# Kernel tuning notes

Hardware: AMD Instinct MI355X
Metric: run time of the kernel (lower is better)

Reference implementation:

```python
import jax, jax.numpy as jnp
import numpy as np
import math

D = 2048
NH = 16
DH = D // NH
LAT = D // 4
B, S = 2, 2048
EPS = 1e-5


def _ln(x, g, b):
    m = jnp.mean(x, axis=-1, keepdims=True)
    v = jnp.mean((x - m) ** 2, axis=-1, keepdims=True)
    return (x - m) * jax.lax.rsqrt(v + EPS) * g + b


def setup_inputs() -> dict:
    key = jax.random.key(0)
    ks = jax.random.split(key, 12)
    p = lambda k, shape: 0.01 * jax.random.normal(k, shape, dtype=jnp.float32)
    return {
        "x": jax.random.normal(ks[0], (B, S, D), dtype=jnp.float32),
        "W_dq": p(ks[1], (D, LAT)),
        "W_uq": p(ks[2], (LAT, D)),
        "q_ln_g": jnp.ones((LAT,), jnp.float32),
        "q_ln_b": jnp.zeros((LAT,), jnp.float32),
        "W_dkv": p(ks[3], (D, LAT)),
        "W_ukv": p(ks[4], (LAT, 2 * D)),
        "kv_ln_g": jnp.ones((LAT,), jnp.float32),
        "kv_ln_b": jnp.zeros((LAT,), jnp.float32),
        "W_o": p(ks[5], (D, D)),
        "norm1_g": jnp.ones((D,), jnp.float32),
        "norm1_b": jnp.zeros((D,), jnp.float32),
        "norm2_g": jnp.ones((D,), jnp.float32),
        "norm2_b": jnp.zeros((D,), jnp.float32),
        "fc1_w": p(ks[6], (4 * D, D)),
        "fc1_b": jnp.zeros((4 * D,), jnp.float32),
        "fc2_w": p(ks[7], (D, 4 * D)),
        "fc2_b": jnp.zeros((D,), jnp.float32),
    }


def reference(x, W_dq, W_uq, q_ln_g, q_ln_b, W_dkv, W_ukv, kv_ln_g, kv_ln_b,
              W_o, norm1_g, norm1_b, norm2_g, norm2_b, fc1_w, fc1_b, fc2_w, fc2_b):
    normed = _ln(x, norm1_g, norm1_b)

    # --- RopelessMLA attention ---
    cq = _ln(normed @ W_dq, q_ln_g, q_ln_b)          # [B,S,LAT]
    Q = cq @ W_uq                                     # [B,S,D]
    ckv = _ln(normed @ W_dkv, kv_ln_g, kv_ln_b)       # [B,S,LAT]
    KV = ckv @ W_ukv                                  # [B,S,2D]
    K, V = KV[..., :D], KV[..., D:]

    q = Q.reshape(B, S, NH, DH)
    k = K.reshape(B, S, NH, DH)
    v = V.reshape(B, S, NH, DH)

    qkt = jnp.einsum("bqhd,bkhd->bhqk", q, k) / math.sqrt(float(DH))
    mask = jnp.tril(jnp.ones((S, S), dtype=qkt.dtype))  # causal, past_length=0
    qkt = qkt * mask
    qkt = jnp.where(qkt == 0.0, -jnp.inf, qkt)  # faithful to original zero->-inf trick
    attn = jax.nn.softmax(qkt, axis=-1)
    o = jnp.einsum("bhqk,bkhd->bqhd", attn, v).reshape(B, S, D)
    mh_x = o @ W_o.T

    x = x + mh_x
    h = _ln(x, norm2_g, norm2_b)
    h = jax.nn.relu(h @ fc1_w.T + fc1_b)
    h = h @ fc2_w.T + fc2_b  # dropout is identity in eval mode
    return x + h
```

## Files before the change

### kernel.cpp

```cpp
#include <hip/hip_runtime.h>
#include <hip/hip_bf16.h>


#define DEVI __device__ __forceinline__

typedef __attribute__((ext_vector_type(8))) short bf16x8;
typedef __attribute__((ext_vector_type(4))) float f32x4;

DEVI unsigned short f2bf(float f) {
  union { float f; unsigned u; } v; v.f = f;
  unsigned r = v.u + 0x7fffu + ((v.u >> 16) & 1u);
  return (unsigned short)(r >> 16);
}

DEVI float bf2f(unsigned short u) {
  union { unsigned u; float f; } v; v.u = ((unsigned)u) << 16;
  return v.f;
}

#define GLDS16(gp, lp)                                              \
  __builtin_amdgcn_global_load_lds(                                 \
      (__attribute__((address_space(1))) void*)(gp),                \
      (__attribute__((address_space(3))) void*)(lp), 16, 0, 0)

#define NEG_INF (-__builtin_inff())

__global__ __launch_bounds__(256) void cast_f32_bf16(
    const float* __restrict__ in, unsigned short* __restrict__ out, long n) {
  long i = ((long)blockIdx.x * 256 + threadIdx.x) * 4;
  if (i >= n) return;
  const float4 v = *reinterpret_cast<const float4*>(in + i);
  ushort4 o;
  o.x = f2bf(v.x); o.y = f2bf(v.y); o.z = f2bf(v.z); o.w = f2bf(v.w);
  *reinterpret_cast<ushort4*>(out + i) = o;
}

__global__ __launch_bounds__(256) void weight_prep(
    const float* __restrict__ W_dq, const float* __restrict__ W_dkv,
    const float* __restrict__ W_uq, const float* __restrict__ W_ukv,
    const float* __restrict__ W_o, unsigned short* __restrict__ dqkv_t,
    unsigned short* __restrict__ uq_t, unsigned short* __restrict__ ukv_t,
    unsigned short* __restrict__ wo_b) {
  __shared__ float tile[32][33];
  const int id = blockIdx.x;
  const int tx = threadIdx.x & 31, ty = threadIdx.x >> 5;
  const float* in;
  unsigned short* out;
  int R, C, bx, by;
  if (id < 1024) {
    in = W_dq; out = dqkv_t; R = 2048; C = 512; bx = id & 15; by = id >> 4;
  } else if (id < 2048) {
    const int t = id - 1024;
    in = W_dkv; out = dqkv_t + 512 * 2048; R = 2048; C = 512; bx = t & 15; by = t >> 4;
  } else if (id < 3072) {
    const int t = id - 2048;
    in = W_uq; out = uq_t; R = 512; C = 2048; bx = t & 63; by = t >> 6;
  } else if (id < 5120) {
    const int t = id - 3072;
    in = W_ukv; out = ukv_t; R = 512; C = 4096; bx = t & 127; by = t >> 7;
  } else {
    const long i = ((long)(id - 5120) * 256 + threadIdx.x) * 4;
    const float4 v = *reinterpret_cast<const float4*>(W_o + i);
    ushort4 o;
    o.x = f2bf(v.x); o.y = f2bf(v.y); o.z = f2bf(v.z); o.w = f2bf(v.w);
    *reinterpret_cast<ushort4*>(wo_b + i) = o;
    return;
  }
  const int c0 = bx * 32, r0 = by * 32;
#pragma unroll
  for (int i = 0; i < 32; i += 8)
    tile[ty + i][tx] = in[(long)(r0 + ty + i) * C + c0 + tx];
  __syncthreads();
#pragma unroll
  for (int i = 0; i < 32; i += 8)
    out[(long)(c0 + ty + i) * R + r0 + tx] = f2bf(tile[tx][ty + i]);
}

__global__ __launch_bounds__(256) void v_transpose(
    const unsigned short* __restrict__ KV, unsigned short* __restrict__ Vt) {
  __shared__ unsigned short sh[32][33];
  const int s0 = blockIdx.x * 32, d0 = blockIdx.y * 32, bh = blockIdx.z;
  const int b = bh >> 4, h = bh & 15;
  const int tx = threadIdx.x & 31, ty = threadIdx.x >> 5;
#pragma unroll
  for (int i = 0; i < 32; i += 8)
    sh[ty + i][tx] = KV[((long)(b * 2048 + s0 + ty + i)) * 4096 + 2048 + h * 128 + d0 + tx];
  __syncthreads();
#pragma unroll
  for (int i = 0; i < 32; i += 8)
    Vt[((long)(bh * 128 + d0 + ty + i)) * 2048 + s0 + tx] = sh[tx][ty + i];
}

DEVI float blockReduceSum(float v) {
  v += __shfl_xor(v, 1);  v += __shfl_xor(v, 2);  v += __shfl_xor(v, 4);
  v += __shfl_xor(v, 8);  v += __shfl_xor(v, 16); v += __shfl_xor(v, 32);
  __shared__ float red[4];
  if ((threadIdx.x & 63) == 0) red[threadIdx.x >> 6] = v;
  __syncthreads();
  v = red[0] + red[1] + red[2] + red[3];
  __syncthreads();
  return v;
}

template <int W>
__global__ __launch_bounds__(256) void layernorm_bf16(
    const float* __restrict__ in, const float* __restrict__ g,
    const float* __restrict__ b, unsigned short* __restrict__ out, int ldin) {
  constexpr int VPT = W / 256;
  const long row = blockIdx.x;
  const float* x = in + row * ldin;
  float v[VPT];
  float s = 0.f;
#pragma unroll
  for (int i = 0; i < VPT; i++) { v[i] = x[threadIdx.x + i * 256]; s += v[i]; }
  s = blockReduceSum(s);
  const float mean = s * (1.0f / W);
  float s2 = 0.f;
#pragma unroll
  for (int i = 0; i < VPT; i++) { float d = v[i] - mean; s2 += d * d; }
  s2 = blockReduceSum(s2);
  const float rstd = rsqrtf(s2 * (1.0f / W) + 1e-5f);
#pragma unroll
  for (int i = 0; i < VPT; i++) {
    const int c = threadIdx.x + i * 256;
    out[row * W + c] = f2bf((v[i] - mean) * rstd * g[c] + b[c]);
  }
}

__global__ __launch_bounds__(256) void ln2x512(
    const float* __restrict__ in, const float* __restrict__ g1,
    const float* __restrict__ b1, const float* __restrict__ g2,
    const float* __restrict__ b2, unsigned short* __restrict__ cq,
    unsigned short* __restrict__ ckv) {
  const long row = blockIdx.x;
  const int tid = threadIdx.x;
  const int half = tid >> 7, lt = tid & 127;
  __shared__ float red[8];
  const float4 v = *reinterpret_cast<const float4*>(in + row * 1024 + half * 512 + lt * 4);
  float s = v.x + v.y + v.z + v.w;
  s += __shfl_xor(s, 1);  s += __shfl_xor(s, 2);  s += __shfl_xor(s, 4);
  s += __shfl_xor(s, 8);  s += __shfl_xor(s, 16); s += __shfl_xor(s, 32);
  if ((tid & 63) == 0) red[tid >> 6] = s;
  __syncthreads();
  const float mean = (red[half * 2] + red[half * 2 + 1]) * (1.f / 512.f);
  const float d0 = v.x - mean, d1 = v.y - mean, d2 = v.z - mean, d3 = v.w - mean;
  float s2 = d0 * d0 + d1 * d1 + d2 * d2 + d3 * d3;
  s2 += __shfl_xor(s2, 1);  s2 += __shfl_xor(s2, 2);  s2 += __shfl_xor(s2, 4);
  s2 += __shfl_xor(s2, 8);  s2 += __shfl_xor(s2, 16); s2 += __shfl_xor(s2, 32);
  if ((tid & 63) == 0) red[4 + (tid >> 6)] = s2;
  __syncthreads();
  const float rstd = rsqrtf((red[4 + half * 2] + red[5 + half * 2]) * (1.f / 512.f) + 1e-5f);
  const float* g = half ? g2 : g1;
  const float* b = half ? b2 : b1;
  const float4 gv = *reinterpret_cast<const float4*>(g + lt * 4);
  const float4 bv = *reinterpret_cast<const float4*>(b + lt * 4);
  ushort4 o;
  o.x = f2bf(d0 * rstd * gv.x + bv.x);
  o.y = f2bf(d1 * rstd * gv.y + bv.y);
  o.z = f2bf(d2 * rstd * gv.z + bv.z);
  o.w = f2bf(d3 * rstd * gv.w + bv.w);
  *reinterpret_cast<ushort4*>((half ? ckv : cq) + row * 512 + lt * 4) = o;
}

__global__ __launch_bounds__(256) void combine_ln(
    const unsigned short* __restrict__ p, const float* __restrict__ xres,
    const float* __restrict__ g, const float* __restrict__ b,
    float* __restrict__ x2, unsigned short* __restrict__ h1, long n) {
  const int c0 = threadIdx.x * 8;
  const long base = (long)blockIdx.x * 2048 + c0;
  float v[8];
  float s = 0.f;
#pragma unroll
  for (int hh = 0; hh < 2; hh++) {
    const long i = base + hh * 4;
    const ushort4 a  = *reinterpret_cast<const ushort4*>(p + i);
    const ushort4 bb = *reinterpret_cast<const ushort4*>(p + n + i);
    const float4 r = *reinterpret_cast<const float4*>(xres + i);
    float4 o;
    o.x = r.x + bf2f(a.x) + bf2f(bb.x);
    o.y = r.y + bf2f(a.y) + bf2f(bb.y);
    o.z = r.z + bf2f(a.z) + bf2f(bb.z);
    o.w = r.w + bf2f(a.w) + bf2f(bb.w);
    *reinterpret_cast<float4*>(x2 + i) = o;
    v[hh * 4 + 0] = o.x; v[hh * 4 + 1] = o.y;
    v[hh * 4 + 2] = o.z; v[hh * 4 + 3] = o.w;
    s += o.x + o.y + o.z + o.w;
  }
  s = blockReduceSum(s);
  const float mean = s * (1.0f / 2048.f);
  float s2 = 0.f;
#pragma unroll
  for (int i = 0; i < 8; i++) { float d = v[i] - mean; s2 += d * d; }
  s2 = blockReduceSum(s2);
  const float rstd = rsqrtf(s2 * (1.0f / 2048.f) + 1e-5f);
#pragma unroll
  for (int hh = 0; hh < 2; hh++) {
    const float4 gv = *reinterpret_cast<const float4*>(g + c0 + hh * 4);
    const float4 bv = *reinterpret_cast<const float4*>(b + c0 + hh * 4);
    ushort4 o;
    o.x = f2bf((v[hh * 4 + 0] - mean) * rstd * gv.x + bv.x);
    o.y = f2bf((v[hh * 4 + 1] - mean) * rstd * gv.y + bv.y);
    o.z = f2bf((v[hh * 4 + 2] - mean) * rstd * gv.z + bv.z);
    o.w = f2bf((v[hh * 4 + 3] - mean) * rstd * gv.w + bv.w);
    *reinterpret_cast<ushort4*>(h1 + base + hh * 4) = o;
  }
}

template <bool BIAS, bool RELU, bool RES, bool OBF16>
__global__ __launch_bounds__(256) void gemm_bt(
    const unsigned short* __restrict__ A, const unsigned short* __restrict__ Bt,
    const float* __restrict__ bias, const float* __restrict__ res,
    void* __restrict__ Cout, int M, int N, int K) {
  __shared__ __align__(16) unsigned short As[2][128 * 32];
  __shared__ __align__(16) unsigned short Bs[2][128 * 32];

  const int m0 = blockIdx.x * 128;
  const int n0 = blockIdx.y * 128;
  const int tid = threadIdx.x;
  const int lane = tid & 63, w = tid >> 6;
  const int wr = (w >> 1) * 64, wc = (w & 1) * 64;
  const int lrow = lane & 15, lk = (lane >> 4) * 8;

  f32x4 acc[4][4] = {};

  const int nt = K >> 5;
  const int r_ = (tid * 8) >> 5;
  const int c_ = (tid * 8) & 31;

#define STAGE(buf, t)                                                        \
  {                                                                          \
    const long k0 = (long)(t) * 32;                                          \
    GLDS16(A + (long)(m0 + r_) * K + k0 + c_, &As[buf][tid * 8]);            \
    GLDS16(A + (long)(m0 + 64 + r_) * K + k0 + c_, &As[buf][2048 + tid * 8]);\
    GLDS16(Bt + (long)(n0 + r_) * K + k0 + c_, &Bs[buf][tid * 8]);           \
    GLDS16(Bt + (long)(n0 + 64 + r_) * K + k0 + c_, &Bs[buf][2048 + tid * 8]);\
  }

  STAGE(0, 0)
  __syncthreads();
  int cur = 0;
  for (int t = 0; t < nt; t++) {
    if (t + 1 < nt) STAGE(cur ^ 1, t + 1)
    bf16x8 fa[4], fb[4];
#pragma unroll
    for (int i = 0; i < 4; i++) {
      fa[i] = *reinterpret_cast<const bf16x8*>(&As[cur][(wr + i * 16 + lrow) * 32 + lk]);
      fb[i] = *reinterpret_cast<const bf16x8*>(&Bs[cur][(wc + i * 16 + lrow) * 32 + lk]);
    }
#pragma unroll
    for (int i = 0; i < 4; i++)
#pragma unroll
      for (int j = 0; j < 4; j++)
        acc[i][j] = __builtin_amdgcn_mfma_f32_16x16x32_bf16(fa[i], fb[j], acc[i][j], 0, 0, 0);
    __syncthreads();
    cur ^= 1;
  }
#undef STAGE

#pragma unroll
  for (int i = 0; i < 4; i++) {
#pragma unroll
    for (int j = 0; j < 4; j++) {
      const int row = m0 + wr + i * 16 + ((lane >> 4) << 2);
      const int col = n0 + wc + j * 16 + lrow;
      float bv = 0.f;
      if (BIAS) bv = bias[col];
#pragma unroll
      for (int r = 0; r < 4; r++) {
        float v = acc[i][j][r];
        const long idx = (long)(row + r) * N + col;
        if (BIAS) v += bv;
        if (RELU) v = fmaxf(v, 0.f);
        if (RES) v += res[idx];
        if (OBF16) ((unsigned short*)Cout)[idx] = f2bf(v);
        else       ((float*)Cout)[idx] = v;
      }
    }
  }
}

template <bool BIAS, bool RELU, bool OBF16>
__global__ __launch_bounds__(512, 1) void gemm256p(
    const unsigned short* __restrict__ A, const unsigned short* __restrict__ Bt,
    const float* __restrict__ bias, void* __restrict__ Cout,
    int M, int N, int lda, int ldb, int kLen, long kOff) {
  __shared__ __align__(16) unsigned short L[2][2][2][256 * 32];

  const int m0 = blockIdx.x * 256, n0 = blockIdx.y * 256;
  const long ka = (long)blockIdx.z * kOff;
  const int tid = threadIdx.x;
  const int lane = tid & 63, w = tid >> 6;
  const int sr = (w >> 2) * 64, sc = (w & 3) * 32;
  const int g = lane >> 4, lrow = lane & 15;
  const int r_ = tid >> 2, s_ = tid & 3;

  f32x4 acc[2][2][4][2] = {};
  const int nt = kLen >> 6;

#define STG1(bb, ab, h, kh, t, P, base0, ld)                                   \
  {                                                                            \
    const long k0 = ka + (long)(t) * 64 + (kh) * 32;                           \
    const int rr = (h) * 128 + r_;                                             \
    GLDS16((P) + (long)((base0) + rr) * (ld) + k0 + ((s_ ^ ((rr >> 1) & 3)) << 3), \
           &L[bb][ab][kh][((h) * 512 + tid) * 8]);                             \
  }
#define STG_A(bb, h, t) STG1(bb, 0, h, 0, t, A, m0, lda) STG1(bb, 0, h, 1, t, A, m0, lda)
#define STG_B(bb, h, t) STG1(bb, 1, h, 0, t, Bt, n0, ldb) STG1(bb, 1, h, 1, t, Bt, n0, ldb)

#define RD_A(fa, bu, a)                                                        \
  _Pragma("unroll")                                                            \
  for (int kh = 0; kh < 2; kh++)                                               \
    _Pragma("unroll")                                                          \
    for (int i = 0; i < 4; i++) {                                              \
      const int rr = (a) * 128 + sr + i * 16 + lrow;                           \
      fa[kh][i] = *reinterpret_cast<const bf16x8*>(                            \
          &L[bu][0][kh][(rr * 4 + (g ^ ((rr >> 1) & 3))) * 8]);                \
    }
#define RD_B(fb, bu, b)                                                        \
  _Pragma("unroll")                                                            \
  for (int kh = 0; kh < 2; kh++)                                               \
    _Pragma("unroll")                                                          \
    for (int j = 0; j < 2; j++) {                                              \
      const int rr = (b) * 128 + sc + j * 16 + lrow;                           \
      fb[kh][j] = *reinterpret_cast<const bf16x8*>(                            \
          &L[bu][1][kh][(rr * 4 + (g ^ ((rr >> 1) & 3))) * 8]);                \
    }

#define PH_MFMA(a, b)                                                          \
  __builtin_amdgcn_s_setprio(1);                                               \
  _Pragma("unroll")                                                            \
  for (int kh = 0; kh < 2; kh++)                                               \
    _Pragma("unroll")                                                          \
    for (int i = 0; i < 4; i++)                                                \
      _Pragma("unroll")                                                        \
      for (int j = 0; j < 2; j++)                                              \
        acc[a][b][i][j] = __builtin_amdgcn_mfma_f32_16x16x32_bf16(             \
            fa[kh][i], fb[kh][j], acc[a][b][i][j], 0, 0, 0);                   \
  __builtin_amdgcn_s_setprio(0);

  STG_A(0, 0, 0) STG_B(0, 0, 0) STG_B(0, 1, 0) STG_A(0, 1, 0)
  asm volatile("s_waitcnt vmcnt(0)\n\ts_barrier" ::: "memory");

  for (int t = 0; t < nt; t++) {
    const int bu = t & 1, bn = bu ^ 1;
    const bool pf = (t + 1 < nt);
    bf16x8 fa[2][4], fb[2][2];
    RD_A(fa, bu, 0)
    RD_B(fb, bu, 0)
    if (pf) STG_A(bn, 0, t + 1)
    PH_MFMA(0, 0)
    RD_B(fb, bu, 1)
    if (pf) STG_B(bn, 1, t + 1)
    PH_MFMA(0, 1)
    if (pf) asm volatile("s_waitcnt vmcnt(4)\n\ts_barrier" ::: "memory");
    else    asm volatile("s_waitcnt vmcnt(0)\n\ts_barrier" ::: "memory");
    RD_A(fa, bu, 1)
    if (pf) STG_B(bn, 0, t + 1)
    PH_MFMA(1, 1)
    RD_B(fb, bu, 0)
    if (pf) STG_A(bn, 1, t + 1)
    PH_MFMA(1, 0)
    if (pf) asm volatile("s_waitcnt vmcnt(2)\n\ts_barrier" ::: "memory");
  }
#undef STG1
#undef STG_A
#undef STG_B
#undef RD_A
#undef RD_B
#undef PH_MFMA

  const long zoff = (long)blockIdx.z * (long)M * (long)N;
#pragma unroll
  for (int a = 0; a < 2; a++) {
#pragma unroll
    for (int b = 0; b < 2; b++) {
#pragma unroll
      for (int i = 0; i < 4; i++) {
#pragma unroll
        for (int j = 0; j < 2; j++) {
          const int row = m0 + a * 128 + sr + i * 16 + g * 4;
          const int col = n0 + b * 128 + sc + j * 16 + lrow;
          float bv = 0.f;
          if (BIAS) bv = bias[col];
#pragma unroll
          for (int r = 0; r < 4; r++) {
            float v = acc[a][b][i][j][r];
            if (BIAS) v += bv;
            if (RELU) v = fmaxf(v, 0.f);
            const long idx = zoff + (long)(row + r) * N + col;
            if (OBF16) ((unsigned short*)Cout)[idx] = f2bf(v);
            else       ((float*)Cout)[idx] = v;
          }
        }
      }
    }
  }
}

template <bool BIAS>
__global__ __launch_bounds__(256) void combine2(
    const unsigned short* __restrict__ p, const float* __restrict__ bias,
    const float* __restrict__ res, float* __restrict__ out, long n) {
  const long i = ((long)blockIdx.x * 256 + threadIdx.x) * 4;
  if (i >= n) return;
  const ushort4 a = *reinterpret_cast<const ushort4*>(p + i);
  const ushort4 b = *reinterpret_cast<const ushort4*>(p + n + i);
  const float4 r = *reinterpret_cast<const float4*>(res + i);
  float4 o;
  o.x = bf2f(a.x) + bf2f(b.x) + r.x;
  o.y = bf2f(a.y) + bf2f(b.y) + r.y;
  o.z = bf2f(a.z) + bf2f(b.z) + r.z;
  o.w = bf2f(a.w) + bf2f(b.w) + r.w;
  if (BIAS) {
    const int col = (int)(i & 2047);
    const float4 bv = *reinterpret_cast<const float4*>(bias + col);
    o.x += bv.x; o.y += bv.y; o.z += bv.z; o.w += bv.w;
  }
  *reinterpret_cast<float4*>(out + i) = o;
}

__global__ __launch_bounds__(256) void flash_attn(
    const unsigned short* __restrict__ Q, const unsigned short* __restrict__ KV,
    const unsigned short* __restrict__ Vt, unsigned short* __restrict__ O) {
  constexpr int S = 2048;
  const int tid = threadIdx.x, lane = tid & 63, w = tid >> 6;
  const int g = lane >> 4, lcol = lane & 15;
  const int wg = blockIdx.x;
  const int x8 = wg & 7, q64 = wg >> 3;
  const int p = q64 & 15, hi = q64 >> 4;
  const int bh = x8 * 4 + hi;
  const int b = bh >> 4, h = bh & 15;
  const long kvrow0 = (long)b * S;
  const int hd0 = h * 128;

  __shared__ __align__(16) unsigned short Kl[64 * 128];
  __shared__ __align__(16) unsigned short Vl[128 * 64];
  __shared__ __align__(16) unsigned short Pl[4 * 16 * 72];

  const float kscale = 0.08838834764831845f * 1.4426950408889634f;

  for (int ti = 0; ti < 2; ti++) {
    const int t = ti ? (31 - p) : p;
    const int qbase = t * 64;
    bf16x8 qf[4];
#pragma unroll
    for (int dc = 0; dc < 4; dc++)
      qf[dc] = *reinterpret_cast<const bf16x8*>(
          Q + (kvrow0 + qbase + w * 16 + lcol) * 2048 + hd0 + dc * 32 + g * 8);
    f32x4 oacc[8] = {};
    float mst[4] = {NEG_INF, NEG_INF, NEG_INF, NEG_INF};
    float lst[4] = {0.f, 0.f, 0.f, 0.f};
    const int nk = t + 1;
    for (int kt = 0; kt < nk; kt++) {
      const int kv0 = kt * 64;
      __syncthreads();
#pragma unroll
      for (int i = 0; i < 4; i++) {
        const int o16 = i * 256 + tid;
        const int kr = o16 >> 4, ks = o16 & 15;
        GLDS16(KV + (kvrow0 + kv0 + kr) * 4096 + hd0 + 8 * (ks ^ (kr & 7)),
               Kl + o16 * 8);
        const int vd = o16 >> 3, vs = o16 & 7;
        GLDS16(Vt + ((long)bh * 128 + vd) * 2048 + kv0 + 8 * (vs ^ (vd & 7)),
               Vl + o16 * 8);
      }
      __syncthreads();
      f32x4 sc[4] = {};
      __builtin_amdgcn_s_setprio(1);
#pragma unroll
      for (int dc = 0; dc < 4; dc++) {
#pragma unroll
        for (int c = 0; c < 4; c++) {
          const bf16x8 kf = *reinterpret_cast<const bf16x8*>(
              Kl + (c * 16 + lcol) * 128 + 8 * ((4 * dc + g) ^ (lcol & 7)));
          sc[c] = __builtin_amdgcn_mfma_f32_16x16x32_bf16(qf[dc], kf, sc[c], 0, 0, 0);
        }
      }
      __builtin_amdgcn_s_setprio(0);
      float s[4][4];
      const int qrow = qbase + w * 16 + g * 4;
      if (kt == nk - 1) {
#pragma unroll
        for (int c = 0; c < 4; c++) {
          const int col = kv0 + c * 16 + lcol;
#pragma unroll
          for (int r = 0; r < 4; r++)
            s[c][r] = (col <= qrow + r) ? sc[c][r] * kscale : NEG_INF;
        }
      } else {
#pragma unroll
        for (int c = 0; c < 4; c++)
#pragma unroll
          for (int r = 0; r < 4; r++) s[c][r] = sc[c][r] * kscale;
      }
      float pm[4];
#pragma unroll
      for (int r = 0; r < 4; r++) {
        float mx = fmaxf(fmaxf(s[0][r], s[1][r]), fmaxf(s[2][r], s[3][r]));
        mx = fmaxf(mx, __shfl_xor(mx, 1));
        mx = fmaxf(mx, __shfl_xor(mx, 2));
        mx = fmaxf(mx, __shfl_xor(mx, 4));
        mx = fmaxf(mx, __shfl_xor(mx, 8));
        pm[r] = mx;
      }
      bool need = false;
#pragma unroll
      for (int r = 0; r < 4; r++) need = need || (pm[r] > mst[r] + 11.5f);
      if (__any(need)) {
#pragma unroll
        for (int r = 0; r < 4; r++) {
          const float mnew = fmaxf(mst[r], pm[r]);
          const float corr = exp2f(mst[r] - mnew);
          mst[r] = mnew;
          lst[r] *= corr;
#pragma unroll
          for (int db = 0; db < 8; db++) oacc[db][r] *= corr;
        }
      }
#pragma unroll
      for (int r = 0; r < 4; r++) {
        float ps = 0.f;
#pragma unroll
        for (int c = 0; c < 4; c++) {
          const float pv = exp2f(s[c][r] - mst[r]);
          Pl[(w * 16 + g * 4 + r) * 72 + c * 16 + lcol] = f2bf(pv);
          ps += pv;
        }
        ps += __shfl_xor(ps, 1); ps += __shfl_xor(ps, 2);
        ps += __shfl_xor(ps, 4); ps += __shfl_xor(ps, 8);
        lst[r] += ps;
      }
      __builtin_amdgcn_s_setprio(1);
#pragma unroll
      for (int kk = 0; kk < 2; kk++) {
        const bf16x8 pf = *reinterpret_cast<const bf16x8*>(
            Pl + (w * 16 + lcol) * 72 + kk * 32 + g * 8);
#pragma unroll
        for (int db = 0; db < 8; db++) {
          const bf16x8 vf = *reinterpret_cast<const bf16x8*>(
              Vl + (db * 16 + lcol) * 64 + 8 * ((4 * kk + g) ^ (lcol & 7)));
          oacc[db] = __builtin_amdgcn_mfma_f32_16x16x32_bf16(pf, vf, oacc[db], 0, 0, 0);
        }
      }
      __builtin_amdgcn_s_setprio(0);
    }
#pragma unroll
    for (int db = 0; db < 8; db++)
#pragma unroll
      for (int r = 0; r < 4; r++) {
        const int qi = qbase + w * 16 + g * 4 + r;
        O[(kvrow0 + qi) * 2048 + hd0 + db * 16 + lcol] = f2bf(oacc[db][r] / lst[r]);
      }
  }
}

extern "C" void kernel_launch(void* const* d_in, const int* in_sizes, int n_in,
                              void* d_out, int out_size, void* d_ws, size_t ws_size,
                              hipStream_t stream) {
  (void)in_sizes; (void)n_in; (void)out_size; (void)ws_size;
  const float* x     = (const float*)d_in[0];
  const float* W_dq  = (const float*)d_in[1];
  const float* W_uq  = (const float*)d_in[2];
  const float* qlng  = (const float*)d_in[3];
  const float* qlnb  = (const float*)d_in[4];
  const float* W_dkv = (const float*)d_in[5];
  const float* W_ukv = (const float*)d_in[6];
  const float* klng  = (const float*)d_in[7];
  const float* klnb  = (const float*)d_in[8];
  const float* W_o   = (const float*)d_in[9];
  const float* n1g   = (const float*)d_in[10];
  const float* n1b   = (const float*)d_in[11];
  const float* n2g   = (const float*)d_in[12];
  const float* n2b   = (const float*)d_in[13];
  const float* fc1w  = (const float*)d_in[14];
  const float* fc1b  = (const float*)d_in[15];
  const float* fc2w  = (const float*)d_in[16];
  const float* fc2b  = (const float*)d_in[17];
  float* out = (float*)d_out;

  char* ws = (char*)d_ws;
  unsigned short* normed = (unsigned short*)(ws + 0);
  unsigned short* Obuf   = (unsigned short*)(ws + 0);
  unsigned short* fc2bb  = (unsigned short*)(ws + 0);
  float*          cqkv_pre = (float*)(ws + 33554432);
  unsigned short* KV       = (unsigned short*)(ws + 33554432);
  unsigned short* fc1bb    = (unsigned short*)(ws + 33554432);
  unsigned short* fc2part  = (unsigned short*)(ws + 33554432);
  unsigned short* cq  = (unsigned short*)(ws + 67108864);
  unsigned short* Qb = (unsigned short*)(ws + 71303168);
  unsigned short* h1 = (unsigned short*)(ws + 71303168);
  unsigned short* ckv = (unsigned short*)(ws + 88080384);
  float* x2           = (float*)(ws + 88080384);
  unsigned short* Vtb    = (unsigned short*)(ws + 121634816);
  unsigned short* wopart = (unsigned short*)(ws + 121634816);
  unsigned short* hmid   = (unsigned short*)(ws + 121634816);
  unsigned short* dqkv_t = (unsigned short*)(ws + 188743680);
  unsigned short* uq_t   = dqkv_t + 2097152;
  unsigned short* ukv_t  = uq_t + 1048576;
  unsigned short* wo_b   = ukv_t + 2097152;

  const dim3 blk(256);
  const dim3 blk8(512);

  weight_prep<<<9216, blk, 0, stream>>>(W_dq, W_dkv, W_uq, W_ukv, W_o,
                                        dqkv_t, uq_t, ukv_t, wo_b);

  layernorm_bf16<2048><<<4096, blk, 0, stream>>>(x, n1g, n1b, normed, 2048);
  gemm_bt<false, false, false, false><<<dim3(32, 8), blk, 0, stream>>>(
      normed, dqkv_t, nullptr, nullptr, cqkv_pre, 4096, 1024, 2048);
  ln2x512<<<4096, blk, 0, stream>>>(cqkv_pre, qlng, qlnb, klng, klnb, cq, ckv);
  gemm_bt<false, false, false, true><<<dim3(32, 16), blk, 0, stream>>>(
      cq, uq_t, nullptr, nullptr, Qb, 4096, 2048, 512);
  gemm256p<false, false, true><<<dim3(16, 16), blk8, 0, stream>>>(
      ckv, ukv_t, nullptr, KV, 4096, 4096, 512, 512, 512, 0);
  v_transpose<<<dim3(64, 4, 32), blk, 0, stream>>>(KV, Vtb);
  flash_attn<<<dim3(512), blk, 0, stream>>>(Qb, KV, Vtb, Obuf);
  cast_f32_bf16<<<8192 * 2048 / 1024, blk, 0, stream>>>(fc1w, fc1bb, 8192L * 2048);
  gemm256p<false, false, true><<<dim3(16, 8, 2), blk8, 0, stream>>>(
      Obuf, wo_b, nullptr, wopart, 4096, 2048, 2048, 2048, 1024, 1024);
  cast_f32_bf16<<<2048 * 8192 / 1024, blk, 0, stream>>>(fc2w, fc2bb, 2048L * 8192);
  combine_ln<<<4096, blk, 0, stream>>>(wopart, x, n2g, n2b, x2, h1, 8388608L);
  gemm256p<true, true, true><<<dim3(16, 32), blk8, 0, stream>>>(
      h1, fc1bb, fc1b, hmid, 4096, 8192, 2048, 2048, 2048, 0);
  gemm256p<false, false, true><<<dim3(16, 8, 2), blk8, 0, stream>>>(
      hmid, fc2bb, nullptr, fc2part, 4096, 2048, 8192, 8192, 4096, 4096);
  combine2<true><<<8192, blk, 0, stream>>>(fc2part, fc2b, x2, out, 8388608L);
}
```

Measured before the change: 549.6 us.

## Split-K the down-projection GEMM and fuse paired-tile flash attention loops

The down-projection GEMM (normed @ [W_dq|W_dkv]) now uses the 256-tile split-K kernel with 4 K-partitions written as bf16 partials. ln2x512 sums those four partials before normalizing, replacing the earlier fp32 single-pass GEMM output. Flash attention now processes its two paired query tiles (p and 31-p) in a single KV loop, so each K/V tile loaded into LDS serves both query tiles instead of being reloaded. This cuts global/LDS traffic and barriers but doubles the register state (two accumulators), which may lower occupancy. It also adds bf16 rounding on the partial sums.

```diff
diff --git a/kernel.cpp b/kernel.cpp
--- a/kernel.cpp
+++ b/kernel.cpp
@@ -128,15 +128,25 @@
 }
 
 __global__ __launch_bounds__(256) void ln2x512(
-    const float* __restrict__ in, const float* __restrict__ g1,
+    const unsigned short* __restrict__ part, const float* __restrict__ g1,
     const float* __restrict__ b1, const float* __restrict__ g2,
     const float* __restrict__ b2, unsigned short* __restrict__ cq,
     unsigned short* __restrict__ ckv) {
+  constexpr long PN = 4096L * 1024;
   const long row = blockIdx.x;
   const int tid = threadIdx.x;
   const int half = tid >> 7, lt = tid & 127;
   __shared__ float red[8];
-  const float4 v = *reinterpret_cast<const float4*>(in + row * 1024 + half * 512 + lt * 4);
+  const long off = row * 1024 + half * 512 + lt * 4;
+  const ushort4 a0 = *reinterpret_cast<const ushort4*>(part + off);
+  const ushort4 a1 = *reinterpret_cast<const ushort4*>(part + PN + off);
+  const ushort4 a2 = *reinterpret_cast<const ushort4*>(part + 2 * PN + off);
+  const ushort4 a3 = *reinterpret_cast<const ushort4*>(part + 3 * PN + off);
+  float4 v;
+  v.x = bf2f(a0.x) + bf2f(a1.x) + bf2f(a2.x) + bf2f(a3.x);
+  v.y = bf2f(a0.y) + bf2f(a1.y) + bf2f(a2.y) + bf2f(a3.y);
+  v.z = bf2f(a0.z) + bf2f(a1.z) + bf2f(a2.z) + bf2f(a3.z);
+  v.w = bf2f(a0.w) + bf2f(a1.w) + bf2f(a2.w) + bf2f(a3.w);
   float s = v.x + v.y + v.z + v.w;
   s += __shfl_xor(s, 1);  s += __shfl_xor(s, 2);  s += __shfl_xor(s, 4);
   s += __shfl_xor(s, 8);  s += __shfl_xor(s, 16); s += __shfl_xor(s, 32);
@@ -432,6 +442,8 @@
   const int b = bh >> 4, h = bh & 15;
   const long kvrow0 = (long)b * S;
   const int hd0 = h * 128;
+  const int tA = p, tB = 31 - p;
+  const int qbaseA = tA * 64, qbaseB = tB * 64;
 
   __shared__ __align__(16) unsigned short Kl[64 * 128];
   __shared__ __align__(16) unsigned short Vl[128 * 64];
@@ -439,119 +451,130 @@
 
   const float kscale = 0.08838834764831845f * 1.4426950408889634f;
 
-  for (int ti = 0; ti < 2; ti++) {
-    const int t = ti ? (31 - p) : p;
-    const int qbase = t * 64;
-    bf16x8 qf[4];
-#pragma unroll
-    for (int dc = 0; dc < 4; dc++)
-      qf[dc] = *reinterpret_cast<const bf16x8*>(
-          Q + (kvrow0 + qbase + w * 16 + lcol) * 2048 + hd0 + dc * 32 + g * 8);
-    f32x4 oacc[8] = {};
-    float mst[4] = {NEG_INF, NEG_INF, NEG_INF, NEG_INF};
-    float lst[4] = {0.f, 0.f, 0.f, 0.f};
-    const int nk = t + 1;
-    for (int kt = 0; kt < nk; kt++) {
-      const int kv0 = kt * 64;
-      __syncthreads();
-#pragma unroll
-      for (int i = 0; i < 4; i++) {
-        const int o16 = i * 256 + tid;
-        const int kr = o16 >> 4, ks = o16 & 15;
-        GLDS16(KV + (kvrow0 + kv0 + kr) * 4096 + hd0 + 8 * (ks ^ (kr & 7)),
-               Kl + o16 * 8);
-        const int vd = o16 >> 3, vs = o16 & 7;
-        GLDS16(Vt + ((long)bh * 128 + vd) * 2048 + kv0 + 8 * (vs ^ (vd & 7)),
-               Vl + o16 * 8);
-      }
-      __syncthreads();
-      f32x4 sc[4] = {};
-      __builtin_amdgcn_s_setprio(1);
-#pragma unroll
-      for (int dc = 0; dc < 4; dc++) {
-#pragma unroll
-        for (int c = 0; c < 4; c++) {
-          const bf16x8 kf = *reinterpret_cast<const bf16x8*>(
-              Kl + (c * 16 + lcol) * 128 + 8 * ((4 * dc + g) ^ (lcol & 7)));
-          sc[c] = __builtin_amdgcn_mfma_f32_16x16x32_bf16(qf[dc], kf, sc[c], 0, 0, 0);
-        }
-      }
-      __builtin_amdgcn_s_setprio(0);
-      float s[4][4];
-      const int qrow = qbase + w * 16 + g * 4;
-      if (kt == nk - 1) {
-#pragma unroll
-        for (int c = 0; c < 4; c++) {
-          const int col = kv0 + c * 16 + lcol;
-#pragma unroll
-          for (int r = 0; r < 4; r++)
-            s[c][r] = (col <= qrow + r) ? sc[c][r] * kscale : NEG_INF;
-        }
-      } else {
-#pragma unroll
-        for (int c = 0; c < 4; c++)
-#pragma unroll
-          for (int r = 0; r < 4; r++) s[c][r] = sc[c][r] * kscale;
-      }
-      float pm[4];
-#pragma unroll
-      for (int r = 0; r < 4; r++) {
-        float mx = fmaxf(fmaxf(s[0][r], s[1][r]), fmaxf(s[2][r], s[3][r]));
-        mx = fmaxf(mx, __shfl_xor(mx, 1));
-        mx = fmaxf(mx, __shfl_xor(mx, 2));
-        mx = fmaxf(mx, __shfl_xor(mx, 4));
-        mx = fmaxf(mx, __shfl_xor(mx, 8));
-        pm[r] = mx;
-      }
-      bool need = false;
-#pragma unroll
-      for (int r = 0; r < 4; r++) need = need || (pm[r] > mst[r] + 11.5f);
-      if (__any(need)) {
-#pragma unroll
-        for (int r = 0; r < 4; r++) {
-          const float mnew = fmaxf(mst[r], pm[r]);
-          const float corr = exp2f(mst[r] - mnew);
-          mst[r] = mnew;
-          lst[r] *= corr;
-#pragma unroll
-          for (int db = 0; db < 8; db++) oacc[db][r] *= corr;
-        }
-      }
-#pragma unroll
-      for (int r = 0; r < 4; r++) {
-        float ps = 0.f;
-#pragma unroll
-        for (int c = 0; c < 4; c++) {
-          const float pv = exp2f(s[c][r] - mst[r]);
-          Pl[(w * 16 + g * 4 + r) * 72 + c * 16 + lcol] = f2bf(pv);
-          ps += pv;
-        }
-        ps += __shfl_xor(ps, 1); ps += __shfl_xor(ps, 2);
-        ps += __shfl_xor(ps, 4); ps += __shfl_xor(ps, 8);
-        lst[r] += ps;
-      }
-      __builtin_amdgcn_s_setprio(1);
-#pragma unroll
-      for (int kk = 0; kk < 2; kk++) {
-        const bf16x8 pf = *reinterpret_cast<const bf16x8*>(
-            Pl + (w * 16 + lcol) * 72 + kk * 32 + g * 8);
-#pragma unroll
-        for (int db = 0; db < 8; db++) {
-          const bf16x8 vf = *reinterpret_cast<const bf16x8*>(
-              Vl + (db * 16 + lcol) * 64 + 8 * ((4 * kk + g) ^ (lcol & 7)));
-          oacc[db] = __builtin_amdgcn_mfma_f32_16x16x32_bf16(pf, vf, oacc[db], 0, 0, 0);
-        }
-      }
-      __builtin_amdgcn_s_setprio(0);
+  bf16x8 qfA[4], qfB[4];
+#pragma unroll
+  for (int dc = 0; dc < 4; dc++) {
+    qfA[dc] = *reinterpret_cast<const bf16x8*>(
+        Q + (kvrow0 + qbaseA + w * 16 + lcol) * 2048 + hd0 + dc * 32 + g * 8);
+    qfB[dc] = *reinterpret_cast<const bf16x8*>(
+        Q + (kvrow0 + qbaseB + w * 16 + lcol) * 2048 + hd0 + dc * 32 + g * 8);
+  }
+  f32x4 oaccA[8] = {}, oaccB[8] = {};
+  float mstA[4] = {NEG_INF, NEG_INF, NEG_INF, NEG_INF};
+  float mstB[4] = {NEG_INF, NEG_INF, NEG_INF, NEG_INF};
+  float lstA[4] = {}, lstB[4] = {};
+
+#define PROC(qf, oacc, mst, lst, qbase, tX)                                    \
+  {                                                                            \
+    f32x4 sc[4] = {};                                                          \
+    __builtin_amdgcn_s_setprio(1);                                             \
+    _Pragma("unroll")                                                          \
+    for (int dc = 0; dc < 4; dc++) {                                           \
+      _Pragma("unroll")                                                        \
+      for (int c = 0; c < 4; c++) {                                            \
+        const bf16x8 kf = *reinterpret_cast<const bf16x8*>(                    \
+            Kl + (c * 16 + lcol) * 128 + 8 * ((4 * dc + g) ^ (lcol & 7)));     \
+        sc[c] = __builtin_amdgcn_mfma_f32_16x16x32_bf16(qf[dc], kf, sc[c], 0, 0, 0); \
+      }                                                                        \
+    }                                                                          \
+    __builtin_amdgcn_s_setprio(0);                                             \
+    float s[4][4];                                                             \
+    const int qrow = (qbase) + w * 16 + g * 4;                                 \
+    if (kt == (tX)) {                                                          \
+      _Pragma("unroll")                                                        \
+      for (int c = 0; c < 4; c++) {                                            \
+        const int col = kv0 + c * 16 + lcol;                                   \
+        _Pragma("unroll")                                                      \
+        for (int r = 0; r < 4; r++)                                            \
+          s[c][r] = (col <= qrow + r) ? sc[c][r] * kscale : NEG_INF;           \
+      }                                                                        \
+    } else {                                                                   \
+      _Pragma("unroll")                                                        \
+      for (int c = 0; c < 4; c++)                                              \
+        _Pragma("unroll")                                                      \
+        for (int r = 0; r < 4; r++) s[c][r] = sc[c][r] * kscale;               \
+    }                                                                          \
+    float pm[4];                                                               \
+    _Pragma("unroll")                                                          \
+    for (int r = 0; r < 4; r++) {                                              \
+      float mx = fmaxf(fmaxf(s[0][r], s[1][r]), fmaxf(s[2][r], s[3][r]));      \
+      mx = fmaxf(mx, __shfl_xor(mx, 1));                                       \
+      mx = fmaxf(mx, __shfl_xor(mx, 2));                                       \
+      mx = fmaxf(mx, __shfl_xor(mx, 4));                                       \
+      mx = fmaxf(mx, __shfl_xor(mx, 8));                                       \
+      pm[r] = mx;                                                              \
+    }                                                                          \
+    bool need = false;                                                         \
+    _Pragma("unroll")                                                          \
+    for (int r = 0; r < 4; r++) need = need || (pm[r] > mst[r] + 11.5f);       \
+    if (__any(need)) {                                                         \
+      _Pragma("unroll")                                                        \
+      for (int r = 0; r < 4; r++) {                                            \
+        const float mnew = fmaxf(mst[r], pm[r]);                               \
+        const float corr = exp2f(mst[r] - mnew);                               \
+        mst[r] = mnew;                                                         \
+        lst[r] *= corr;                                                        \
+        _Pragma("unroll")                                                      \
+        for (int db = 0; db < 8; db++) oacc[db][r] *= corr;                    \
+      }                                                                        \
+    }                                                                          \
+    _Pragma("unroll")                                                          \
+    for (int r = 0; r < 4; r++) {                                              \
+      float ps = 0.f;                                                          \
+      _Pragma("unroll")                                                        \
+      for (int c = 0; c < 4; c++) {                                            \
+        const float pv = exp2f(s[c][r] - mst[r]);                              \
+        Pl[(w * 16 + g * 4 + r) * 72 + c * 16 + lcol] = f2bf(pv);              \
+        ps += pv;                                                              \
+      }                                                                        \
+      ps += __shfl_xor(ps, 1); ps += __shfl_xor(ps, 2);                        \
+      ps += __shfl_xor(ps, 4); ps += __shfl_xor(ps, 8);                        \
+      lst[r] += ps;                                                            \
+    }                                                                          \
+    __builtin_amdgcn_s_setprio(1);                                             \
+    _Pragma("unroll")                                                          \
+    for (int kk = 0; kk < 2; kk++) {                                           \
+      const bf16x8 pf = *reinterpret_cast<const bf16x8*>(                      \
+          Pl + (w * 16 + lcol) * 72 + kk * 32 + g * 8);                        \
+      _Pragma("unroll")                                                        \
+      for (int db = 0; db < 8; db++) {                                         \
+        const bf16x8 vf = *reinterpret_cast<const bf16x8*>(                    \
+            Vl + (db * 16 + lcol) * 64 + 8 * ((4 * kk + g) ^ (lcol & 7)));     \
+        oacc[db] = __builtin_amdgcn_mfma_f32_16x16x32_bf16(pf, vf, oacc[db], 0, 0, 0); \
+      }                                                                        \
+    }                                                                          \
+    __builtin_amdgcn_s_setprio(0);                                             \
+  }
+
+  const int nk = tB + 1;
+  for (int kt = 0; kt < nk; kt++) {
+    const int kv0 = kt * 64;
+    __syncthreads();
+#pragma unroll
+    for (int i = 0; i < 4; i++) {
+      const int o16 = i * 256 + tid;
+      const int kr = o16 >> 4, ks = o16 & 15;
+      GLDS16(KV + (kvrow0 + kv0 + kr) * 4096 + hd0 + 8 * (ks ^ (kr & 7)),
+             Kl + o16 * 8);
+      const int vd = o16 >> 3, vs = o16 & 7;
+      GLDS16(Vt + ((long)bh * 128 + vd) * 2048 + kv0 + 8 * (vs ^ (vd & 7)),
+             Vl + o16 * 8);
     }
-#pragma unroll
-    for (int db = 0; db < 8; db++)
-#pragma unroll
-      for (int r = 0; r < 4; r++) {
-        const int qi = qbase + w * 16 + g * 4 + r;
-        O[(kvrow0 + qi) * 2048 + hd0 + db * 16 + lcol] = f2bf(oacc[db][r] / lst[r]);
-      }
-  }
+    __syncthreads();
+    PROC(qfB, oaccB, mstB, lstB, qbaseB, tB)
+    if (kt <= tA) PROC(qfA, oaccA, mstA, lstA, qbaseA, tA)
+  }
+#undef PROC
+
+#pragma unroll
+  for (int db = 0; db < 8; db++)
+#pragma unroll
+    for (int r = 0; r < 4; r++) {
+      const int qiA = qbaseA + w * 16 + g * 4 + r;
+      const int qiB = qbaseB + w * 16 + g * 4 + r;
+      O[(kvrow0 + qiA) * 2048 + hd0 + db * 16 + lcol] = f2bf(oaccA[db][r] / lstA[r]);
+      O[(kvrow0 + qiB) * 2048 + hd0 + db * 16 + lcol] = f2bf(oaccB[db][r] / lstB[r]);
+    }
 }
 
 extern "C" void kernel_launch(void* const* d_in, const int* in_sizes, int n_in,
@@ -582,10 +605,10 @@
   unsigned short* normed = (unsigned short*)(ws + 0);
   unsigned short* Obuf   = (unsigned short*)(ws + 0);
   unsigned short* fc2bb  = (unsigned short*)(ws + 0);
-  float*          cqkv_pre = (float*)(ws + 33554432);
-  unsigned short* KV       = (unsigned short*)(ws + 33554432);
-  unsigned short* fc1bb    = (unsigned short*)(ws + 33554432);
-  unsigned short* fc2part  = (unsigned short*)(ws + 33554432);
+  unsigned short* cqkv_part = (unsigned short*)(ws + 33554432);
+  unsigned short* KV        = (unsigned short*)(ws + 33554432);
+  unsigned short* fc1bb     = (unsigned short*)(ws + 33554432);
+  unsigned short* fc2part   = (unsigned short*)(ws + 33554432);
   unsigned short* cq  = (unsigned short*)(ws + 67108864);
   unsigned short* Qb = (unsigned short*)(ws + 71303168);
   unsigned short* h1 = (unsigned short*)(ws + 71303168);
@@ -606,9 +629,9 @@
                                         dqkv_t, uq_t, ukv_t, wo_b);
 
   layernorm_bf16<2048><<<4096, blk, 0, stream>>>(x, n1g, n1b, normed, 2048);
-  gemm_bt<false, false, false, false><<<dim3(32, 8), blk, 0, stream>>>(
-      normed, dqkv_t, nullptr, nullptr, cqkv_pre, 4096, 1024, 2048);
-  ln2x512<<<4096, blk, 0, stream>>>(cqkv_pre, qlng, qlnb, klng, klnb, cq, ckv);
+  gemm256p<false, false, true><<<dim3(16, 4, 4), blk8, 0, stream>>>(
+      normed, dqkv_t, nullptr, cqkv_part, 4096, 1024, 2048, 2048, 512, 512);
+  ln2x512<<<4096, blk, 0, stream>>>(cqkv_part, qlng, qlnb, klng, klnb, cq, ckv);
   gemm_bt<false, false, false, true><<<dim3(32, 16), blk, 0, stream>>>(
       cq, uq_t, nullptr, nullptr, Qb, 4096, 2048, 512);
   gemm256p<false, false, true><<<dim3(16, 16), blk8, 0, stream>>>(
```

Result: slower. 588.5 us (+7.1%).
